# Kernel optimization log

Hardware: AMD Instinct MI355X
Metric: run time of the kernel (lower is better)

Reference implementation:

```python
import jax, jax.numpy as jnp
import numpy as np

N2, T, E, D = 512, 4096, 512, 256  # G2 nodes, G1 type nodes, G1 entity nodes, embed dim


def setup_inputs() -> dict:
    key = jax.random.key(0)
    k = jax.random.split(key, 6)
    return {
        "all_node_embedding": jax.random.normal(k[0], (N2 + T, D), jnp.float32),
        "W2": jax.random.normal(k[1], (N2, N2, D), jnp.float32),
        "R2": jax.random.normal(k[2], (N2, N2, D), jnp.float32),
        "A1": jax.random.randint(k[3], (T, T), 0, 2, jnp.int32),
        "A2": jax.random.randint(k[4], (E, T), 0, 2, jnp.int32),
        "A3": jax.random.randint(k[5], (T, E), 0, 2, jnp.int32),
    }


def reference(all_node_embedding, W2, R2, A1, A2, A3):
    emb = all_node_embedding
    dt = emb.dtype
    n2, t = W2.shape[0], A1.shape[0]
    start = n2
    e = A2.shape[0]

    # --- G2_update: broadcast emb[i] over rows j, weight, add relation, sum over i ---
    x2 = emb[:n2]                                   # [N2, D]
    new2 = jnp.einsum("id,jid->jd", x2, W2) + R2.sum(1) + x2
    emb = emb.at[:n2].set(new2)

    # --- G1_sub1_update: every column filled -> full sum broadcast, degree-normalized gate ---
    sub = emb[start:start + t]                      # [T, D]
    S = sub.sum(0)                                  # [D], same for every row
    new1 = sub + S[None, :]
    deg1 = 1.0 + (A1 != 0).sum(1).astype(dt)        # [T] row nonzero counts + 1
    new1 = new1 * (1.0 - S[None, :] / deg1[:, None])
    emb = emb.at[start:start + t].set(new1)

    # --- G1_sub2: specific (entities) -> common (types); non-edges contribute ones ---
    A2f = (A2 != 0).astype(dt)                      # [E, T]
    spec = emb[:e]                                  # [E, D]
    deg2 = A2f.sum(0)                               # [T]
    msg2 = A2f.T @ spec + (e - deg2)[:, None]       # ones-filled background
    new_common = emb[start:start + t] + msg2
    emb = emb.at[start:start + t].set(new_common)

    # --- G1_sub3: common (types) -> specific (entities), degree-normalized gate ---
    A3f = (A3 != 0).astype(dt)                      # [T, E]
    deg3 = A3f.sum(0)                               # [E] column nonzero counts
    msg3 = A3f.T @ new_common + (t - deg3)[:, None]
    sum_arr = 1.0 + deg3                            # [E]
    new_spec = emb[:e] * (1.0 - msg3 / sum_arr[:, None])
    emb = emb.at[:e].set(new_spec)
    return emb
```

## Files before the change

kernel.cpp:

```cpp
#include <hip/hip_runtime.h>
#include <stdint.h>

#define DN 256
#define N2C 512
#define TC 4096
#define EC 512

#define B_K1_END  512
#define B_K2A_END 576
#define B_K2B_END 1088
#define B_P2_END  1600
#define B_P3_END  2112

__global__ __launch_bounds__(512) void prep_fused(
    const float* __restrict__ emb, const float* __restrict__ W2,
    const float* __restrict__ R2, const int* __restrict__ A1,
    const int* __restrict__ A2, const int* __restrict__ A3,
    float* __restrict__ out, float* __restrict__ S,
    float* __restrict__ deg1, uint32_t* __restrict__ PT2,
    uint32_t* __restrict__ PT3)
{
    __shared__ uint32_t ldsb[64][65];
    __shared__ float4 red[8][64];
    const int bid = blockIdx.x;
    const int tid = threadIdx.x;

    if (bid < B_K1_END) {
        const int d4  = tid & 63;
        const int grp = tid >> 6;
        const int j   = bid;
        const float4* W = (const float4*)(W2 + (size_t)j * N2C * DN);
        const float4* R = (const float4*)(R2 + (size_t)j * N2C * DN);
        const float4* X = (const float4*)emb;

        float ax = 0.f, ay = 0.f, az = 0.f, aw = 0.f;
        const int i0 = grp * 64;
        #pragma unroll 4
        for (int i = i0; i < i0 + 64; ++i) {
            float4 w = W[i * 64 + d4];
            float4 r = R[i * 64 + d4];
            float4 x = X[i * 64 + d4];
            ax += x.x * w.x + r.x;
            ay += x.y * w.y + r.y;
            az += x.z * w.z + r.z;
            aw += x.w * w.w + r.w;
        }
        float4 mine; mine.x = ax; mine.y = ay; mine.z = az; mine.w = aw;
        red[grp][d4] = mine;
        __syncthreads();
        if (grp == 0) {
            float sx = 0.f, sy = 0.f, sz = 0.f, sw = 0.f;
            #pragma unroll
            for (int g = 0; g < 8; ++g) {
                float4 v = red[g][d4];
                sx += v.x; sy += v.y; sz += v.z; sw += v.w;
            }
            float4 x = X[j * 64 + d4];
            float4 o;
            o.x = sx + x.x; o.y = sy + x.y; o.z = sz + x.z; o.w = sw + x.w;
            ((float4*)out)[j * 64 + d4] = o;
        }
    } else if (bid < B_K2A_END) {
        const int b = bid - B_K1_END;
        const int d = tid & 255;
        const int h = tid >> 8;
        const float* base = emb + (size_t)N2C * DN;
        const int r0 = b * 64 + h * 32;
        float s = 0.f;
        #pragma unroll 4
        for (int r = r0; r < r0 + 32; ++r) s += base[(size_t)r * DN + d];
        atomicAdd(&S[d], s);
    } else if (bid < B_K2B_END) {
        const int b    = bid - B_K2A_END;
        const int row  = b * 8 + (tid >> 6);
        const int lane = tid & 63;
        const int4* p = (const int4*)(A1 + (size_t)row * TC);
        int cnt = 0;
        #pragma unroll
        for (int k = 0; k < 16; ++k) {
            int4 v = p[k * 64 + lane];
            cnt += (v.x != 0) + (v.y != 0) + (v.z != 0) + (v.w != 0);
        }
        #pragma unroll
        for (int off = 32; off > 0; off >>= 1) cnt += __shfl_down(cnt, off, 64);
        if (lane == 0) deg1[row] = 1.0f + (float)cnt;
    } else if (bid < B_P2_END) {
        const int bb = bid - B_K2B_END;
        const int e0 = (bb & 7) * 64;
        const int t0 = (bb >> 3) * 64;
        const int tx = tid & 63;
        const int ty = tid >> 6;
        #pragma unroll
        for (int k = 0; k < 8; ++k) {
            int el = ty * 8 + k;
            ldsb[el][tx] = (A2[(size_t)(e0 + el) * TC + t0 + tx] != 0) ? 1u : 0u;
        }
        __syncthreads();
        if (tid < 128) {
            const int tl = tid & 63;
            const int w  = tid >> 6;
            uint32_t bits = 0;
            #pragma unroll
            for (int b = 0; b < 32; ++b) bits |= ldsb[w * 32 + b][tl] << b;
            PT2[(size_t)(t0 + tl) * 16 + (e0 >> 5) + w] = bits;
        }
    } else {
        const int bb = bid - B_P2_END;
        const int t0 = (bb >> 3) * 64;
        const int e0 = (bb & 7) * 64;
        const int ex = tid & 63;
        const int ty = tid >> 6;
        #pragma unroll
        for (int k = 0; k < 8; ++k) {
            int tl = ty * 8 + k;
            ldsb[tl][ex] = (A3[(size_t)(t0 + tl) * EC + e0 + ex] != 0) ? 1u : 0u;
        }
        __syncthreads();
        if (tid < 128) {
            const int el = tid & 63;
            const int w  = tid >> 6;
            uint32_t bits = 0;
            #pragma unroll
            for (int b = 0; b < 32; ++b) bits |= ldsb[w * 32 + b][el] << b;
            PT3[(size_t)(e0 + el) * 128 + (t0 >> 5) + w] = bits;
        }
    }
}

__global__ __launch_bounds__(256) void k3_dense(
    const float* __restrict__ emb, const uint32_t* __restrict__ PT2,
    const float* __restrict__ S, const float* __restrict__ deg1,
    float* out)
{
    const int d4 = threadIdx.x & 63;
    const int tg = threadIdx.x >> 6;
    const int t0 = blockIdx.x * 16 + tg * 4;
    const float4* spec = (const float4*)out;
    const uint32_t* pt = PT2 + (size_t)t0 * 16;

    float4 a0 = {0,0,0,0}, a1 = {0,0,0,0}, a2 = {0,0,0,0}, a3 = {0,0,0,0};
    int c0 = 0, c1 = 0, c2 = 0, c3 = 0;

    for (int ec = 0; ec < 16; ++ec) {
        const uint32_t w0 = pt[ec];
        const uint32_t w1 = pt[16 + ec];
        const uint32_t w2 = pt[32 + ec];
        const uint32_t w3 = pt[48 + ec];
        c0 += __popc(w0); c1 += __popc(w1); c2 += __popc(w2); c3 += __popc(w3);
        const float4* sp = spec + (size_t)ec * 32 * 64 + d4;
        #pragma unroll
        for (int b = 0; b < 32; ++b) {
            float4 v = sp[b * 64];
            float m0 = (float)((w0 >> b) & 1u);
            float m1 = (float)((w1 >> b) & 1u);
            float m2 = (float)((w2 >> b) & 1u);
            float m3 = (float)((w3 >> b) & 1u);
            a0.x = fmaf(m0, v.x, a0.x); a0.y = fmaf(m0, v.y, a0.y);
            a0.z = fmaf(m0, v.z, a0.z); a0.w = fmaf(m0, v.w, a0.w);
            a1.x = fmaf(m1, v.x, a1.x); a1.y = fmaf(m1, v.y, a1.y);
            a1.z = fmaf(m1, v.z, a1.z); a1.w = fmaf(m1, v.w, a1.w);
            a2.x = fmaf(m2, v.x, a2.x); a2.y = fmaf(m2, v.y, a2.y);
            a2.z = fmaf(m2, v.z, a2.z); a2.w = fmaf(m2, v.w, a2.w);
            a3.x = fmaf(m3, v.x, a3.x); a3.y = fmaf(m3, v.y, a3.y);
            a3.z = fmaf(m3, v.z, a3.z); a3.w = fmaf(m3, v.w, a3.w);
        }
    }

    const float4 Sv = ((const float4*)S)[d4];
#define K3_EPI(ak, ck, kk) { \
    const int t = t0 + kk; \
    const float inv = 1.0f / deg1[t]; \
    const float addc = (float)(EC - ck); \
    const float4 sub = ((const float4*)emb)[(size_t)(N2C + t) * 64 + d4]; \
    float4 o; \
    o.x = (sub.x + Sv.x) * (1.0f - Sv.x * inv) + ak.x + addc; \
    o.y = (sub.y + Sv.y) * (1.0f - Sv.y * inv) + ak.y + addc; \
    o.z = (sub.z + Sv.z) * (1.0f - Sv.z * inv) + ak.z + addc; \
    o.w = (sub.w + Sv.w) * (1.0f - Sv.w * inv) + ak.w + addc; \
    ((float4*)out)[(size_t)(N2C + t) * 64 + d4] = o; }
    K3_EPI(a0, c0, 0)
    K3_EPI(a1, c1, 1)
    K3_EPI(a2, c2, 2)
    K3_EPI(a3, c3, 3)
#undef K3_EPI
}

__global__ __launch_bounds__(256) void k4_part(
    const uint32_t* __restrict__ PT3, const float* __restrict__ out,
    float* __restrict__ P)
{
    const int d4    = threadIdx.x & 63;
    const int es    = threadIdx.x >> 6;
    const int etile = blockIdx.x >> 2;
    const int chunk = blockIdx.x & 3;
    const int e0 = etile * 8 + es * 2;
    const float4* nc = (const float4*)(out + (size_t)N2C * DN);
    const uint32_t* p0 = PT3 + (size_t)e0 * 128 + chunk * 32;
    const uint32_t* p1 = p0 + 128;

    float4 a0 = {0,0,0,0}, a1 = {0,0,0,0};
    for (int w = 0; w < 32; ++w) {
        const uint32_t m0 = p0[w];
        const uint32_t m1 = p1[w];
        const float4* np = nc + (size_t)((chunk * 32 + w) * 32) * 64 + d4;
        #pragma unroll
        for (int b = 0; b < 32; ++b) {
            float4 v = np[b * 64];
            float f0 = (float)((m0 >> b) & 1u);
            float f1 = (float)((m1 >> b) & 1u);
            a0.x = fmaf(f0, v.x, a0.x); a0.y = fmaf(f0, v.y, a0.y);
            a0.z = fmaf(f0, v.z, a0.z); a0.w = fmaf(f0, v.w, a0.w);
            a1.x = fmaf(f1, v.x, a1.x); a1.y = fmaf(f1, v.y, a1.y);
            a1.z = fmaf(f1, v.z, a1.z); a1.w = fmaf(f1, v.w, a1.w);
        }
    }
    float4* Pp = (float4*)P;
    Pp[((size_t)chunk * EC + e0) * 64 + d4]     = a0;
    Pp[((size_t)chunk * EC + e0 + 1) * 64 + d4] = a1;
}

__global__ __launch_bounds__(256) void k4_fin(
    const uint32_t* __restrict__ PT3, const float* __restrict__ P,
    float* out)
{
    const int d4 = threadIdx.x & 63;
    const int es = threadIdx.x >> 6;
    const int e  = blockIdx.x * 4 + es;
    const float4* Pp = (const float4*)P;

    float4 s0 = Pp[((size_t)0 * EC + e) * 64 + d4];
    float4 s1 = Pp[((size_t)1 * EC + e) * 64 + d4];
    float4 s2 = Pp[((size_t)2 * EC + e) * 64 + d4];
    float4 s3 = Pp[((size_t)3 * EC + e) * 64 + d4];
    float4 s;
    s.x = s0.x + s1.x + s2.x + s3.x;
    s.y = s0.y + s1.y + s2.y + s3.y;
    s.z = s0.z + s1.z + s2.z + s3.z;
    s.w = s0.w + s1.w + s2.w + s3.w;

    int c = __popc(PT3[(size_t)e * 128 + 2 * d4]) +
            __popc(PT3[(size_t)e * 128 + 2 * d4 + 1]);
    #pragma unroll
    for (int off = 32; off > 0; off >>= 1) c += __shfl_xor(c, off, 64);

    const float msg_add = (float)(TC - c);
    const float inv = 1.0f / (1.0f + (float)c);
    float4 cur = ((const float4*)out)[(size_t)e * 64 + d4];
    float4 o;
    o.x = cur.x * (1.0f - (s.x + msg_add) * inv);
    o.y = cur.y * (1.0f - (s.y + msg_add) * inv);
    o.z = cur.z * (1.0f - (s.z + msg_add) * inv);
    o.w = cur.w * (1.0f - (s.w + msg_add) * inv);
    ((float4*)out)[(size_t)e * 64 + d4] = o;
}

extern "C" void kernel_launch(void* const* d_in, const int* in_sizes, int n_in,
                              void* d_out, int out_size, void* d_ws, size_t ws_size,
                              hipStream_t stream) {
    const float* emb = (const float*)d_in[0];
    const float* W2  = (const float*)d_in[1];
    const float* R2  = (const float*)d_in[2];
    const int*   A1  = (const int*)d_in[3];
    const int*   A2  = (const int*)d_in[4];
    const int*   A3  = (const int*)d_in[5];
    float* out = (float*)d_out;

    float*    S    = (float*)d_ws;
    float*    deg1 = S + DN;
    uint32_t* PT2  = (uint32_t*)(deg1 + TC);
    uint32_t* PT3  = PT2 + (size_t)TC * 16;
    float*    P    = (float*)(PT3 + (size_t)EC * 128);

    hipMemsetAsync(d_ws, 0, DN * sizeof(float), stream);

    prep_fused<<<B_P3_END, 512, 0, stream>>>(emb, W2, R2, A1, A2, A3,
                                             out, S, deg1, PT2, PT3);
    k3_dense<<<TC / 16, 256, 0, stream>>>(emb, PT2, S, deg1, out);
    k4_part<<<256, 256, 0, stream>>>(PT3, out, P);
    k4_fin<<<EC / 4, 256, 0, stream>>>(PT3, P, out);
}
```

Before: 213.5 us.

## Interleave prep jobs across blocks and widen register tiles in dense kernels

The fused prep kernel now interleaves its four job types (W2/R2 reduction, A1 degree count, A2 and A3 bit-packing) block by block, so the bandwidth-heavy W2/R2 blocks are spread across the grid instead of all running first. The W2 loop gets a different thread-to-address mapping and separate accumulators for the multiply and the R2 sum, and the shared-memory buffers are overlaid in one array. k3_dense and k4_part each keep 8 accumulator rows per thread instead of 4 or 2, so every loaded vector is reused more. The cost is higher register pressure and fewer blocks (128 and 64), which can reduce occupancy and leave parts of the GPU idle.

```diff
diff --git a/kernel.cpp b/kernel.cpp
--- a/kernel.cpp
+++ b/kernel.cpp
@@ -6,11 +6,8 @@
 #define TC 4096
 #define EC 512
 
-#define B_K1_END  512
-#define B_K2A_END 576
-#define B_K2B_END 1088
-#define B_P2_END  1600
-#define B_P3_END  2112
+#define B_MIX_END 2048
+#define B_TOTAL   2112
 
 __global__ __launch_bounds__(512) void prep_fused(
     const float* __restrict__ emb, const float* __restrict__ W2,
@@ -20,48 +17,112 @@
     float* __restrict__ deg1, uint32_t* __restrict__ PT2,
     uint32_t* __restrict__ PT3)
 {
-    __shared__ uint32_t ldsb[64][65];
-    __shared__ float4 red[8][64];
+    __shared__ __align__(16) char smem[64 * 65 * 4];
+    uint32_t (*ldsb)[65] = (uint32_t (*)[65])smem;
+    float4   (*red)[64]  = (float4 (*)[64])smem;
+
     const int bid = blockIdx.x;
     const int tid = threadIdx.x;
 
-    if (bid < B_K1_END) {
-        const int d4  = tid & 63;
-        const int grp = tid >> 6;
-        const int j   = bid;
-        const float4* W = (const float4*)(W2 + (size_t)j * N2C * DN);
-        const float4* R = (const float4*)(R2 + (size_t)j * N2C * DN);
-        const float4* X = (const float4*)emb;
-
-        float ax = 0.f, ay = 0.f, az = 0.f, aw = 0.f;
-        const int i0 = grp * 64;
-        #pragma unroll 4
-        for (int i = i0; i < i0 + 64; ++i) {
-            float4 w = W[i * 64 + d4];
-            float4 r = R[i * 64 + d4];
-            float4 x = X[i * 64 + d4];
-            ax += x.x * w.x + r.x;
-            ay += x.y * w.y + r.y;
-            az += x.z * w.z + r.z;
-            aw += x.w * w.w + r.w;
-        }
-        float4 mine; mine.x = ax; mine.y = ay; mine.z = az; mine.w = aw;
-        red[grp][d4] = mine;
-        __syncthreads();
-        if (grp == 0) {
-            float sx = 0.f, sy = 0.f, sz = 0.f, sw = 0.f;
-            #pragma unroll
-            for (int g = 0; g < 8; ++g) {
-                float4 v = red[g][d4];
-                sx += v.x; sy += v.y; sz += v.z; sw += v.w;
-            }
-            float4 x = X[j * 64 + d4];
-            float4 o;
-            o.x = sx + x.x; o.y = sy + x.y; o.z = sz + x.z; o.w = sw + x.w;
-            ((float4*)out)[j * 64 + d4] = o;
-        }
-    } else if (bid < B_K2A_END) {
-        const int b = bid - B_K1_END;
+    if (bid < B_MIX_END) {
+        const int job = bid & 3;
+        const int sub = bid >> 2;
+
+        if (job == 0) {
+            const int d4  = tid & 63;
+            const int grp = tid >> 6;
+            const int j   = sub;
+            const float4* W = (const float4*)(W2 + (size_t)j * N2C * DN);
+            const float4* R = (const float4*)(R2 + (size_t)j * N2C * DN);
+            const float4* X = (const float4*)emb;
+
+            const int base = grp * 64 + d4;
+            float4 aw = {0.f, 0.f, 0.f, 0.f};
+            float4 ar = {0.f, 0.f, 0.f, 0.f};
+            #pragma unroll 4
+            for (int it = 0; it < 64; ++it) {
+                const int idx = it * 512 + base;
+                float4 w = W[idx];
+                float4 r = R[idx];
+                float4 x = X[idx];
+                aw.x = fmaf(x.x, w.x, aw.x);
+                aw.y = fmaf(x.y, w.y, aw.y);
+                aw.z = fmaf(x.z, w.z, aw.z);
+                aw.w = fmaf(x.w, w.w, aw.w);
+                ar.x += r.x; ar.y += r.y; ar.z += r.z; ar.w += r.w;
+            }
+            float4 mine;
+            mine.x = aw.x + ar.x; mine.y = aw.y + ar.y;
+            mine.z = aw.z + ar.z; mine.w = aw.w + ar.w;
+            red[grp][d4] = mine;
+            __syncthreads();
+            if (grp == 0) {
+                float sx = 0.f, sy = 0.f, sz = 0.f, sw = 0.f;
+                #pragma unroll
+                for (int g = 0; g < 8; ++g) {
+                    float4 v = red[g][d4];
+                    sx += v.x; sy += v.y; sz += v.z; sw += v.w;
+                }
+                float4 x = X[j * 64 + d4];
+                float4 o;
+                o.x = sx + x.x; o.y = sy + x.y;
+                o.z = sz + x.z; o.w = sw + x.w;
+                ((float4*)out)[j * 64 + d4] = o;
+            }
+        } else if (job == 1) {
+            const int row  = sub * 8 + (tid >> 6);
+            const int lane = tid & 63;
+            const int4* p = (const int4*)(A1 + (size_t)row * TC);
+            int cnt = 0;
+            #pragma unroll
+            for (int k = 0; k < 16; ++k) {
+                int4 v = p[k * 64 + lane];
+                cnt += (v.x != 0) + (v.y != 0) + (v.z != 0) + (v.w != 0);
+            }
+            #pragma unroll
+            for (int off = 32; off > 0; off >>= 1) cnt += __shfl_down(cnt, off, 64);
+            if (lane == 0) deg1[row] = 1.0f + (float)cnt;
+        } else if (job == 2) {
+            const int e0 = (sub & 7) * 64;
+            const int t0 = (sub >> 3) * 64;
+            const int tx = tid & 63;
+            const int ty = tid >> 6;
+            #pragma unroll
+            for (int k = 0; k < 8; ++k) {
+                int el = ty * 8 + k;
+                ldsb[el][tx] = (A2[(size_t)(e0 + el) * TC + t0 + tx] != 0) ? 1u : 0u;
+            }
+            __syncthreads();
+            if (tid < 128) {
+                const int tl = tid & 63;
+                const int w  = tid >> 6;
+                uint32_t bits = 0;
+                #pragma unroll
+                for (int b = 0; b < 32; ++b) bits |= ldsb[w * 32 + b][tl] << b;
+                PT2[(size_t)(t0 + tl) * 16 + (e0 >> 5) + w] = bits;
+            }
+        } else {
+            const int t0 = (sub >> 3) * 64;
+            const int e0 = (sub & 7) * 64;
+            const int ex = tid & 63;
+            const int ty = tid >> 6;
+            #pragma unroll
+            for (int k = 0; k < 8; ++k) {
+                int tl = ty * 8 + k;
+                ldsb[tl][ex] = (A3[(size_t)(t0 + tl) * EC + e0 + ex] != 0) ? 1u : 0u;
+            }
+            __syncthreads();
+            if (tid < 128) {
+                const int el = tid & 63;
+                const int w  = tid >> 6;
+                uint32_t bits = 0;
+                #pragma unroll
+                for (int b = 0; b < 32; ++b) bits |= ldsb[w * 32 + b][el] << b;
+                PT3[(size_t)(e0 + el) * 128 + (t0 >> 5) + w] = bits;
+            }
+        }
+    } else {
+        const int b = bid - B_MIX_END;
         const int d = tid & 255;
         const int h = tid >> 8;
         const float* base = emb + (size_t)N2C * DN;
@@ -70,60 +131,6 @@
         #pragma unroll 4
         for (int r = r0; r < r0 + 32; ++r) s += base[(size_t)r * DN + d];
         atomicAdd(&S[d], s);
-    } else if (bid < B_K2B_END) {
-        const int b    = bid - B_K2A_END;
-        const int row  = b * 8 + (tid >> 6);
-        const int lane = tid & 63;
-        const int4* p = (const int4*)(A1 + (size_t)row * TC);
-        int cnt = 0;
-        #pragma unroll
-        for (int k = 0; k < 16; ++k) {
-            int4 v = p[k * 64 + lane];
-            cnt += (v.x != 0) + (v.y != 0) + (v.z != 0) + (v.w != 0);
-        }
-        #pragma unroll
-        for (int off = 32; off > 0; off >>= 1) cnt += __shfl_down(cnt, off, 64);
-        if (lane == 0) deg1[row] = 1.0f + (float)cnt;
-    } else if (bid < B_P2_END) {
-        const int bb = bid - B_K2B_END;
-        const int e0 = (bb & 7) * 64;
-        const int t0 = (bb >> 3) * 64;
-        const int tx = tid & 63;
-        const int ty = tid >> 6;
-        #pragma unroll
-        for (int k = 0; k < 8; ++k) {
-            int el = ty * 8 + k;
-            ldsb[el][tx] = (A2[(size_t)(e0 + el) * TC + t0 + tx] != 0) ? 1u : 0u;
-        }
-        __syncthreads();
-        if (tid < 128) {
-            const int tl = tid & 63;
-            const int w  = tid >> 6;
-            uint32_t bits = 0;
-            #pragma unroll
-            for (int b = 0; b < 32; ++b) bits |= ldsb[w * 32 + b][tl] << b;
-            PT2[(size_t)(t0 + tl) * 16 + (e0 >> 5) + w] = bits;
-        }
-    } else {
-        const int bb = bid - B_P2_END;
-        const int t0 = (bb >> 3) * 64;
-        const int e0 = (bb & 7) * 64;
-        const int ex = tid & 63;
-        const int ty = tid >> 6;
-        #pragma unroll
-        for (int k = 0; k < 8; ++k) {
-            int tl = ty * 8 + k;
-            ldsb[tl][ex] = (A3[(size_t)(t0 + tl) * EC + e0 + ex] != 0) ? 1u : 0u;
-        }
-        __syncthreads();
-        if (tid < 128) {
-            const int el = tid & 63;
-            const int w  = tid >> 6;
-            uint32_t bits = 0;
-            #pragma unroll
-            for (int b = 0; b < 32; ++b) bits |= ldsb[w * 32 + b][el] << b;
-            PT3[(size_t)(e0 + el) * 128 + (t0 >> 5) + w] = bits;
-        }
     }
 }
 
@@ -134,55 +141,50 @@
 {
     const int d4 = threadIdx.x & 63;
     const int tg = threadIdx.x >> 6;
-    const int t0 = blockIdx.x * 16 + tg * 4;
+    const int t0 = blockIdx.x * 32 + tg * 8;
     const float4* spec = (const float4*)out;
-    const uint32_t* pt = PT2 + (size_t)t0 * 16;
-
-    float4 a0 = {0,0,0,0}, a1 = {0,0,0,0}, a2 = {0,0,0,0}, a3 = {0,0,0,0};
-    int c0 = 0, c1 = 0, c2 = 0, c3 = 0;
+
+    float4 acc[8];
+    int cnt[8];
+    #pragma unroll
+    for (int k = 0; k < 8; ++k) { acc[k] = make_float4(0.f,0.f,0.f,0.f); cnt[k] = 0; }
 
     for (int ec = 0; ec < 16; ++ec) {
-        const uint32_t w0 = pt[ec];
-        const uint32_t w1 = pt[16 + ec];
-        const uint32_t w2 = pt[32 + ec];
-        const uint32_t w3 = pt[48 + ec];
-        c0 += __popc(w0); c1 += __popc(w1); c2 += __popc(w2); c3 += __popc(w3);
+        uint32_t m[8];
+        #pragma unroll
+        for (int k = 0; k < 8; ++k) {
+            m[k] = PT2[(size_t)(t0 + k) * 16 + ec];
+            cnt[k] += __popc(m[k]);
+        }
         const float4* sp = spec + (size_t)ec * 32 * 64 + d4;
         #pragma unroll
         for (int b = 0; b < 32; ++b) {
             float4 v = sp[b * 64];
-            float m0 = (float)((w0 >> b) & 1u);
-            float m1 = (float)((w1 >> b) & 1u);
-            float m2 = (float)((w2 >> b) & 1u);
-            float m3 = (float)((w3 >> b) & 1u);
-            a0.x = fmaf(m0, v.x, a0.x); a0.y = fmaf(m0, v.y, a0.y);
-            a0.z = fmaf(m0, v.z, a0.z); a0.w = fmaf(m0, v.w, a0.w);
-            a1.x = fmaf(m1, v.x, a1.x); a1.y = fmaf(m1, v.y, a1.y);
-            a1.z = fmaf(m1, v.z, a1.z); a1.w = fmaf(m1, v.w, a1.w);
-            a2.x = fmaf(m2, v.x, a2.x); a2.y = fmaf(m2, v.y, a2.y);
-            a2.z = fmaf(m2, v.z, a2.z); a2.w = fmaf(m2, v.w, a2.w);
-            a3.x = fmaf(m3, v.x, a3.x); a3.y = fmaf(m3, v.y, a3.y);
-            a3.z = fmaf(m3, v.z, a3.z); a3.w = fmaf(m3, v.w, a3.w);
+            #pragma unroll
+            for (int k = 0; k < 8; ++k) {
+                float f = (float)((m[k] >> b) & 1u);
+                acc[k].x = fmaf(f, v.x, acc[k].x);
+                acc[k].y = fmaf(f, v.y, acc[k].y);
+                acc[k].z = fmaf(f, v.z, acc[k].z);
+                acc[k].w = fmaf(f, v.w, acc[k].w);
+            }
         }
     }
 
     const float4 Sv = ((const float4*)S)[d4];
-#define K3_EPI(ak, ck, kk) { \
-    const int t = t0 + kk; \
-    const float inv = 1.0f / deg1[t]; \
-    const float addc = (float)(EC - ck); \
-    const float4 sub = ((const float4*)emb)[(size_t)(N2C + t) * 64 + d4]; \
-    float4 o; \
-    o.x = (sub.x + Sv.x) * (1.0f - Sv.x * inv) + ak.x + addc; \
-    o.y = (sub.y + Sv.y) * (1.0f - Sv.y * inv) + ak.y + addc; \
-    o.z = (sub.z + Sv.z) * (1.0f - Sv.z * inv) + ak.z + addc; \
-    o.w = (sub.w + Sv.w) * (1.0f - Sv.w * inv) + ak.w + addc; \
-    ((float4*)out)[(size_t)(N2C + t) * 64 + d4] = o; }
-    K3_EPI(a0, c0, 0)
-    K3_EPI(a1, c1, 1)
-    K3_EPI(a2, c2, 2)
-    K3_EPI(a3, c3, 3)
-#undef K3_EPI
+    #pragma unroll
+    for (int k = 0; k < 8; ++k) {
+        const int t = t0 + k;
+        const float inv = 1.0f / deg1[t];
+        const float addc = (float)(EC - cnt[k]);
+        const float4 sub = ((const float4*)emb)[(size_t)(N2C + t) * 64 + d4];
+        float4 o;
+        o.x = (sub.x + Sv.x) * (1.0f - Sv.x * inv) + acc[k].x + addc;
+        o.y = (sub.y + Sv.y) * (1.0f - Sv.y * inv) + acc[k].y + addc;
+        o.z = (sub.z + Sv.z) * (1.0f - Sv.z * inv) + acc[k].z + addc;
+        o.w = (sub.w + Sv.w) * (1.0f - Sv.w * inv) + acc[k].w + addc;
+        ((float4*)out)[(size_t)(N2C + t) * 64 + d4] = o;
+    }
 }
 
 __global__ __launch_bounds__(256) void k4_part(
@@ -193,30 +195,36 @@
     const int es    = threadIdx.x >> 6;
     const int etile = blockIdx.x >> 2;
     const int chunk = blockIdx.x & 3;
-    const int e0 = etile * 8 + es * 2;
+    const int e0 = etile * 32 + es * 8;
     const float4* nc = (const float4*)(out + (size_t)N2C * DN);
-    const uint32_t* p0 = PT3 + (size_t)e0 * 128 + chunk * 32;
-    const uint32_t* p1 = p0 + 128;
-
-    float4 a0 = {0,0,0,0}, a1 = {0,0,0,0};
+
+    float4 acc[8];
+    #pragma unroll
+    for (int k = 0; k < 8; ++k) acc[k] = make_float4(0.f,0.f,0.f,0.f);
+
     for (int w = 0; w < 32; ++w) {
-        const uint32_t m0 = p0[w];
-        const uint32_t m1 = p1[w];
+        uint32_t m[8];
+        #pragma unroll
+        for (int k = 0; k < 8; ++k)
+            m[k] = PT3[(size_t)(e0 + k) * 128 + chunk * 32 + w];
         const float4* np = nc + (size_t)((chunk * 32 + w) * 32) * 64 + d4;
         #pragma unroll
         for (int b = 0; b < 32; ++b) {
             float4 v = np[b * 64];
-            float f0 = (float)((m0 >> b) & 1u);
-            float f1 = (float)((m1 >> b) & 1u);
-            a0.x = fmaf(f0, v.x, a0.x); a0.y = fmaf(f0, v.y, a0.y);
-            a0.z = fmaf(f0, v.z, a0.z); a0.w = fmaf(f0, v.w, a0.w);
-            a1.x = fmaf(f1, v.x, a1.x); a1.y = fmaf(f1, v.y, a1.y);
-            a1.z = fmaf(f1, v.z, a1.z); a1.w = fmaf(f1, v.w, a1.w);
+            #pragma unroll
+            for (int k = 0; k < 8; ++k) {
+                float f = (float)((m[k] >> b) & 1u);
+                acc[k].x = fmaf(f, v.x, acc[k].x);
+                acc[k].y = fmaf(f, v.y, acc[k].y);
+                acc[k].z = fmaf(f, v.z, acc[k].z);
+                acc[k].w = fmaf(f, v.w, acc[k].w);
+            }
         }
     }
     float4* Pp = (float4*)P;
-    Pp[((size_t)chunk * EC + e0) * 64 + d4]     = a0;
-    Pp[((size_t)chunk * EC + e0 + 1) * 64 + d4] = a1;
+    #pragma unroll
+    for (int k = 0; k < 8; ++k)
+        Pp[((size_t)chunk * EC + e0 + k) * 64 + d4] = acc[k];
 }
 
 __global__ __launch_bounds__(256) void k4_fin(
@@ -273,9 +281,9 @@
 
     hipMemsetAsync(d_ws, 0, DN * sizeof(float), stream);
 
-    prep_fused<<<B_P3_END, 512, 0, stream>>>(emb, W2, R2, A1, A2, A3,
-                                             out, S, deg1, PT2, PT3);
-    k3_dense<<<TC / 16, 256, 0, stream>>>(emb, PT2, S, deg1, out);
-    k4_part<<<256, 256, 0, stream>>>(PT3, out, P);
+    prep_fused<<<B_TOTAL, 512, 0, stream>>>(emb, W2, R2, A1, A2, A3,
+                                            out, S, deg1, PT2, PT3);
+    k3_dense<<<TC / 32, 256, 0, stream>>>(emb, PT2, S, deg1, out);
+    k4_part<<<64, 256, 0, stream>>>(PT3, out, P);
     k4_fin<<<EC / 4, 256, 0, stream>>>(PT3, P, out);
 }
```

Measured after the change: 511.0 us. +139.3%, slower.

## Consolidate adjacency prep blocks and retile k4 partial sums to 4 entities

Applied to the files above, without the earlier changes.

The auxiliary work in the fused prep kernel (A1 degree counts, A2/A3 bit-packing, column sums) is merged into 256 uniform blocks, each doing several tasks in sequence, and the shared memory for the reduction and transpose buffers is aliased into one region. k4_part now has each wavefront accumulate 4 entities over 8 chunks instead of 2 entities over 4 chunks, so every loaded embedding row is reused more, and k4_fin sums 8 partials. The aim is to cut block count and scheduling imbalance and raise reuse in the gather, at the cost of more serial work per block and more partial-sum traffic.

```diff
diff --git a/kernel.cpp b/kernel.cpp
--- a/kernel.cpp
+++ b/kernel.cpp
@@ -6,11 +6,8 @@
 #define TC 4096
 #define EC 512
 
-#define B_K1_END  512
-#define B_K2A_END 576
-#define B_K2B_END 1088
-#define B_P2_END  1600
-#define B_P3_END  2112
+#define B_K1 512
+#define B_A  256
 
 __global__ __launch_bounds__(512) void prep_fused(
     const float* __restrict__ emb, const float* __restrict__ W2,
@@ -20,12 +17,14 @@
     float* __restrict__ deg1, uint32_t* __restrict__ PT2,
     uint32_t* __restrict__ PT3)
 {
-    __shared__ uint32_t ldsb[64][65];
-    __shared__ float4 red[8][64];
+    __shared__ __align__(16) char smem[64 * 65 * 4];
+    uint32_t (*ldsb)[65] = (uint32_t (*)[65])smem;
+    float4   (*red)[64]  = (float4 (*)[64])smem;
+
     const int bid = blockIdx.x;
     const int tid = threadIdx.x;
 
-    if (bid < B_K1_END) {
+    if (bid < B_K1) {
         const int d4  = tid & 63;
         const int grp = tid >> 6;
         const int j   = bid;
@@ -60,69 +59,85 @@
             o.x = sx + x.x; o.y = sy + x.y; o.z = sz + x.z; o.w = sw + x.w;
             ((float4*)out)[j * 64 + d4] = o;
         }
-    } else if (bid < B_K2A_END) {
-        const int b = bid - B_K1_END;
-        const int d = tid & 255;
-        const int h = tid >> 8;
-        const float* base = emb + (size_t)N2C * DN;
-        const int r0 = b * 64 + h * 32;
-        float s = 0.f;
-        #pragma unroll 4
-        for (int r = r0; r < r0 + 32; ++r) s += base[(size_t)r * DN + d];
-        atomicAdd(&S[d], s);
-    } else if (bid < B_K2B_END) {
-        const int b    = bid - B_K2A_END;
-        const int row  = b * 8 + (tid >> 6);
-        const int lane = tid & 63;
-        const int4* p = (const int4*)(A1 + (size_t)row * TC);
-        int cnt = 0;
+    } else {
+        const int ab = bid - B_K1;
+
+        {
+            const int lane = tid & 63;
+            #pragma unroll
+            for (int it = 0; it < 2; ++it) {
+                const int row = ab * 16 + it * 8 + (tid >> 6);
+                const int4* p = (const int4*)(A1 + (size_t)row * TC);
+                int cnt = 0;
+                #pragma unroll
+                for (int k = 0; k < 16; ++k) {
+                    int4 v = p[k * 64 + lane];
+                    cnt += (v.x != 0) + (v.y != 0) + (v.z != 0) + (v.w != 0);
+                }
+                #pragma unroll
+                for (int off = 32; off > 0; off >>= 1)
+                    cnt += __shfl_down(cnt, off, 64);
+                if (lane == 0) deg1[row] = 1.0f + (float)cnt;
+            }
+        }
+
         #pragma unroll
-        for (int k = 0; k < 16; ++k) {
-            int4 v = p[k * 64 + lane];
-            cnt += (v.x != 0) + (v.y != 0) + (v.z != 0) + (v.w != 0);
-        }
+        for (int pt = 0; pt < 2; ++pt) {
+            const int sub = ab * 2 + pt;
+            const int e0 = (sub & 7) * 64;
+            const int t0 = (sub >> 3) * 64;
+            const int tx = tid & 63;
+            const int ty = tid >> 6;
+            #pragma unroll
+            for (int k = 0; k < 8; ++k) {
+                int el = ty * 8 + k;
+                ldsb[el][tx] = (A2[(size_t)(e0 + el) * TC + t0 + tx] != 0) ? 1u : 0u;
+            }
+            __syncthreads();
+            if (tid < 128) {
+                const int tl = tid & 63;
+                const int w  = tid >> 6;
+                uint32_t bits = 0;
+                #pragma unroll
+                for (int b = 0; b < 32; ++b) bits |= ldsb[w * 32 + b][tl] << b;
+                PT2[(size_t)(t0 + tl) * 16 + (e0 >> 5) + w] = bits;
+            }
+            __syncthreads();
+        }
+
         #pragma unroll
-        for (int off = 32; off > 0; off >>= 1) cnt += __shfl_down(cnt, off, 64);
-        if (lane == 0) deg1[row] = 1.0f + (float)cnt;
-    } else if (bid < B_P2_END) {
-        const int bb = bid - B_K2B_END;
-        const int e0 = (bb & 7) * 64;
-        const int t0 = (bb >> 3) * 64;
-        const int tx = tid & 63;
-        const int ty = tid >> 6;
-        #pragma unroll
-        for (int k = 0; k < 8; ++k) {
-            int el = ty * 8 + k;
-            ldsb[el][tx] = (A2[(size_t)(e0 + el) * TC + t0 + tx] != 0) ? 1u : 0u;
-        }
-        __syncthreads();
-        if (tid < 128) {
-            const int tl = tid & 63;
-            const int w  = tid >> 6;
-            uint32_t bits = 0;
-            #pragma unroll
-            for (int b = 0; b < 32; ++b) bits |= ldsb[w * 32 + b][tl] << b;
-            PT2[(size_t)(t0 + tl) * 16 + (e0 >> 5) + w] = bits;
-        }
-    } else {
-        const int bb = bid - B_P2_END;
-        const int t0 = (bb >> 3) * 64;
-        const int e0 = (bb & 7) * 64;
-        const int ex = tid & 63;
-        const int ty = tid >> 6;
-        #pragma unroll
-        for (int k = 0; k < 8; ++k) {
-            int tl = ty * 8 + k;
-            ldsb[tl][ex] = (A3[(size_t)(t0 + tl) * EC + e0 + ex] != 0) ? 1u : 0u;
-        }
-        __syncthreads();
-        if (tid < 128) {
-            const int el = tid & 63;
-            const int w  = tid >> 6;
-            uint32_t bits = 0;
-            #pragma unroll
-            for (int b = 0; b < 32; ++b) bits |= ldsb[w * 32 + b][el] << b;
-            PT3[(size_t)(e0 + el) * 128 + (t0 >> 5) + w] = bits;
+        for (int pt = 0; pt < 2; ++pt) {
+            const int sub = ab * 2 + pt;
+            const int t0 = (sub >> 3) * 64;
+            const int e0 = (sub & 7) * 64;
+            const int ex = tid & 63;
+            const int ty = tid >> 6;
+            #pragma unroll
+            for (int k = 0; k < 8; ++k) {
+                int tl = ty * 8 + k;
+                ldsb[tl][ex] = (A3[(size_t)(t0 + tl) * EC + e0 + ex] != 0) ? 1u : 0u;
+            }
+            __syncthreads();
+            if (tid < 128) {
+                const int el = tid & 63;
+                const int w  = tid >> 6;
+                uint32_t bits = 0;
+                #pragma unroll
+                for (int b = 0; b < 32; ++b) bits |= ldsb[w * 32 + b][el] << b;
+                PT3[(size_t)(e0 + el) * 128 + (t0 >> 5) + w] = bits;
+            }
+            __syncthreads();
+        }
+
+        {
+            const int d = tid & 255;
+            const int h = tid >> 8;
+            const float* base = emb + (size_t)N2C * DN;
+            const int r0 = ab * 16 + h * 8;
+            float s = 0.f;
+            #pragma unroll
+            for (int r = r0; r < r0 + 8; ++r) s += base[(size_t)r * DN + d];
+            atomicAdd(&S[d], s);
         }
     }
 }
@@ -191,32 +206,41 @@
 {
     const int d4    = threadIdx.x & 63;
     const int es    = threadIdx.x >> 6;
-    const int etile = blockIdx.x >> 2;
-    const int chunk = blockIdx.x & 3;
-    const int e0 = etile * 8 + es * 2;
+    const int etile = blockIdx.x >> 3;
+    const int chunk = blockIdx.x & 7;
+    const int e0 = etile * 16 + es * 4;
     const float4* nc = (const float4*)(out + (size_t)N2C * DN);
-    const uint32_t* p0 = PT3 + (size_t)e0 * 128 + chunk * 32;
-    const uint32_t* p1 = p0 + 128;
-
-    float4 a0 = {0,0,0,0}, a1 = {0,0,0,0};
-    for (int w = 0; w < 32; ++w) {
-        const uint32_t m0 = p0[w];
-        const uint32_t m1 = p1[w];
-        const float4* np = nc + (size_t)((chunk * 32 + w) * 32) * 64 + d4;
+
+    float4 a0 = {0,0,0,0}, a1 = {0,0,0,0}, a2 = {0,0,0,0}, a3 = {0,0,0,0};
+
+    for (int w = 0; w < 16; ++w) {
+        const uint32_t m0 = PT3[(size_t)(e0 + 0) * 128 + chunk * 16 + w];
+        const uint32_t m1 = PT3[(size_t)(e0 + 1) * 128 + chunk * 16 + w];
+        const uint32_t m2 = PT3[(size_t)(e0 + 2) * 128 + chunk * 16 + w];
+        const uint32_t m3 = PT3[(size_t)(e0 + 3) * 128 + chunk * 16 + w];
+        const float4* np = nc + (size_t)((chunk * 16 + w) * 32) * 64 + d4;
         #pragma unroll
         for (int b = 0; b < 32; ++b) {
             float4 v = np[b * 64];
             float f0 = (float)((m0 >> b) & 1u);
             float f1 = (float)((m1 >> b) & 1u);
+            float f2 = (float)((m2 >> b) & 1u);
+            float f3 = (float)((m3 >> b) & 1u);
             a0.x = fmaf(f0, v.x, a0.x); a0.y = fmaf(f0, v.y, a0.y);
             a0.z = fmaf(f0, v.z, a0.z); a0.w = fmaf(f0, v.w, a0.w);
             a1.x = fmaf(f1, v.x, a1.x); a1.y = fmaf(f1, v.y, a1.y);
             a1.z = fmaf(f1, v.z, a1.z); a1.w = fmaf(f1, v.w, a1.w);
+            a2.x = fmaf(f2, v.x, a2.x); a2.y = fmaf(f2, v.y, a2.y);
+            a2.z = fmaf(f2, v.z, a2.z); a2.w = fmaf(f2, v.w, a2.w);
+            a3.x = fmaf(f3, v.x, a3.x); a3.y = fmaf(f3, v.y, a3.y);
+            a3.z = fmaf(f3, v.z, a3.z); a3.w = fmaf(f3, v.w, a3.w);
         }
     }
     float4* Pp = (float4*)P;
-    Pp[((size_t)chunk * EC + e0) * 64 + d4]     = a0;
+    Pp[((size_t)chunk * EC + e0 + 0) * 64 + d4] = a0;
     Pp[((size_t)chunk * EC + e0 + 1) * 64 + d4] = a1;
+    Pp[((size_t)chunk * EC + e0 + 2) * 64 + d4] = a2;
+    Pp[((size_t)chunk * EC + e0 + 3) * 64 + d4] = a3;
 }
 
 __global__ __launch_bounds__(256) void k4_fin(
@@ -228,15 +252,12 @@
     const int e  = blockIdx.x * 4 + es;
     const float4* Pp = (const float4*)P;
 
-    float4 s0 = Pp[((size_t)0 * EC + e) * 64 + d4];
-    float4 s1 = Pp[((size_t)1 * EC + e) * 64 + d4];
-    float4 s2 = Pp[((size_t)2 * EC + e) * 64 + d4];
-    float4 s3 = Pp[((size_t)3 * EC + e) * 64 + d4];
-    float4 s;
-    s.x = s0.x + s1.x + s2.x + s3.x;
-    s.y = s0.y + s1.y + s2.y + s3.y;
-    s.z = s0.z + s1.z + s2.z + s3.z;
-    s.w = s0.w + s1.w + s2.w + s3.w;
+    float4 s = {0.f, 0.f, 0.f, 0.f};
+    #pragma unroll
+    for (int c = 0; c < 8; ++c) {
+        float4 v = Pp[((size_t)c * EC + e) * 64 + d4];
+        s.x += v.x; s.y += v.y; s.z += v.z; s.w += v.w;
+    }
 
     int c = __popc(PT3[(size_t)e * 128 + 2 * d4]) +
             __popc(PT3[(size_t)e * 128 + 2 * d4 + 1]);
@@ -273,8 +294,8 @@
 
     hipMemsetAsync(d_ws, 0, DN * sizeof(float), stream);
 
-    prep_fused<<<B_P3_END, 512, 0, stream>>>(emb, W2, R2, A1, A2, A3,
-                                             out, S, deg1, PT2, PT3);
+    prep_fused<<<B_K1 + B_A, 512, 0, stream>>>(emb, W2, R2, A1, A2, A3,
+                                               out, S, deg1, PT2, PT3);
     k3_dense<<<TC / 16, 256, 0, stream>>>(emb, PT2, S, deg1, out);
     k4_part<<<256, 256, 0, stream>>>(PT3, out, P);
     k4_fin<<<EC / 4, 256, 0, stream>>>(PT3, P, out);
```

Measured after the change: 215.9 us. About the same (+1.1%).
